# Kernel tuning notes

Hardware: AMD Instinct MI355X
Metric: run time of the kernel (lower is better)

## Reference

```python
import jax, jax.numpy as jnp
import numpy as np

BATCH, MAXLEN, EMB, HID = 64, 512, 1024, 1024


def setup_inputs() -> dict:
    key = jax.random.key(0)
    k1, k2, k3, k4 = jax.random.split(key, 4)
    stdv = 1.0 / np.sqrt(HID)  # matches reset_parameters uniform(-stdv, stdv)
    x = jax.random.normal(k1, (BATCH, MAXLEN, EMB), dtype=jnp.float32)
    lengths = jax.random.randint(k2, (BATCH,), 1, MAXLEN + 1)
    W_ih = jax.random.uniform(k3, (4 * HID, EMB), jnp.float32, -stdv, stdv)
    W_hh = jax.random.uniform(k4, (4 * HID, HID), jnp.float32, -stdv, stdv)
    return {"x": x, "lengths": lengths, "W_ih": W_ih, "W_hh": W_hh}


def reference(x, lengths, W_ih, W_hh):
    B, T, D = x.shape
    H = W_hh.shape[1]
    # length_to_mask: (B, T) float mask
    masks = (jnp.arange(T)[None, :] < lengths[:, None]).astype(x.dtype)
    # Hoist the input projection (no sequential dependency): (B, T, 4H)
    gi_all = jnp.einsum('btd,gd->btg', x, W_ih)

    def step(carry, inp):
        h, c = carry
        gi, m, is_init = inp  # gi: (B,4H), m: (B,), is_init: scalar bool
        gh = h @ W_hh.T  # (B, 4H)
        i_i, i_f, i_g, i_o = jnp.split(gi, 4, axis=1)
        h_i, h_f, h_g, h_o = jnp.split(gh, 4, axis=1)
        gx_i = jax.nn.sigmoid(i_i); fx_i = gx_i * (1 - gx_i)
        gx_f = jax.nn.sigmoid(i_f)
        gx_o = jax.nn.sigmoid(i_o); fx_o = gx_o * (1 - gx_o)
        gx_c = jnp.tanh(i_g);       fx_c = 1 - gx_c ** 2
        g_c = gx_i * gx_c
        g_c_tanh = jnp.tanh(g_c)
        g_h = gx_o * g_c_tanh
        Bt = gx_f * c
        Dt = gx_c * fx_i * h_i + gx_i * fx_c * h_g
        sech2 = 1 - g_c_tanh ** 2
        Et = gx_o * sech2 * gx_f * c
        Ft = gx_o * sech2 * Dt + fx_o * g_c_tanh * h_o
        h_new = Et + Ft + jnp.where(is_init, g_h, jnp.zeros_like(g_h))
        c_new = Bt + Dt + jnp.where(is_init, g_c, jnp.zeros_like(g_c))
        mm = m[:, None]
        h2 = h_new * mm + h * (1 - mm)
        c2 = c_new * mm + c * (1 - mm)
        return (h2, c2), h2

    h0 = jnp.zeros((B, H), x.dtype)
    c0 = jnp.zeros((B, H), x.dtype)
    xs = (gi_all.transpose(1, 0, 2),  # (T, B, 4H)
          masks.T,                    # (T, B)
          jnp.arange(T) == 0)         # (T,) is_initial flags
    (h_final, c_final), seq = jax.lax.scan(step, (h0, c0), xs)
    f_seq = seq.transpose(1, 0, 2)  # (B, T, H)
    return f_seq, h_final
```

## Files before the change

### kernel.cpp

```cpp
#include <hip/hip_runtime.h>
#include <math.h>

#define BB_  64
#define TT_  512
#define DD_  1024
#define HH_  1024

__device__ __forceinline__ unsigned short bf_rte(float f) {
    unsigned u = __float_as_uint(f);
    return (unsigned short)((u + 0x7FFFu + ((u >> 16) & 1u)) >> 16);
}
__device__ __forceinline__ void bf_split(float f, unsigned short& h,
                                         unsigned short& l) {
    unsigned u = __float_as_uint(f);
    unsigned r = (u + 0x7FFFu + ((u >> 16) & 1u)) >> 16;
    h = (unsigned short)r;
    l = bf_rte(f - __uint_as_float(r << 16));
}
__device__ __forceinline__ uint4 pack8(float4 v0, float4 v1, bool lo) {
    float f[8] = {v0.x, v0.y, v0.z, v0.w, v1.x, v1.y, v1.z, v1.w};
    unsigned short s[8];
#pragma unroll
    for (int j = 0; j < 8; ++j) {
        unsigned short h, l;
        bf_split(f[j], h, l);
        s[j] = lo ? l : h;
    }
    uint4 r;
    r.x = (unsigned)s[0] | ((unsigned)s[1] << 16);
    r.y = (unsigned)s[2] | ((unsigned)s[3] << 16);
    r.z = (unsigned)s[4] | ((unsigned)s[5] << 16);
    r.w = (unsigned)s[6] | ((unsigned)s[7] << 16);
    return r;
}

typedef short bf16x8 __attribute__((ext_vector_type(8)));
typedef float f32x4 __attribute__((ext_vector_type(4)));

__global__ __launch_bounds__(256)
void gemm_bf16x3(const float* __restrict__ X,
                 const float* __restrict__ Wih,
                 float* __restrict__ C)
{
    __shared__ unsigned short As[128 * 64];
    __shared__ unsigned short Bs[128 * 64];
    const int tid = threadIdx.x;
    const size_t m0 = (size_t)blockIdx.y * 128;
    const size_t n0 = (size_t)blockIdx.x * 128;
    const int wave = tid >> 6, lane = tid & 63;
    const int wr = wave >> 1, wc = wave & 1;

    f32x4 acc[4][4];
#pragma unroll
    for (int i = 0; i < 4; ++i)
#pragma unroll
        for (int j = 0; j < 4; ++j)
#pragma unroll
            for (int r = 0; r < 4; ++r) acc[i][j][r] = 0.f;

    for (int ks = 0; ks < 48; ++ks) {
        const int seg = ks >> 4;
        const int kph = (ks & 15) << 6;
        const bool aLo = (seg == 2);
        const bool bLo = (seg == 1);
        uint4 ua[4], ub[4];
#pragma unroll
        for (int c = 0; c < 4; ++c) {
            int chunk = tid + c * 256;
            int row = chunk >> 3, kc = chunk & 7;
            const float* ap = X + (m0 + row) * 1024 + kph + kc * 8;
            ua[c] = pack8(*(const float4*)ap, *(const float4*)(ap + 4), aLo);
            const float* bp = Wih + (n0 + row) * 1024 + kph + kc * 8;
            ub[c] = pack8(*(const float4*)bp, *(const float4*)(bp + 4), bLo);
        }
        __syncthreads();
#pragma unroll
        for (int c = 0; c < 4; ++c) {
            int chunk = tid + c * 256;
            int row = chunk >> 3, kc = chunk & 7;
            int sc = kc ^ (row & 7);
            *(uint4*)&As[row * 64 + sc * 8] = ua[c];
            *(uint4*)&Bs[row * 64 + sc * 8] = ub[c];
        }
        __syncthreads();
#pragma unroll
        for (int kk = 0; kk < 64; kk += 32) {
            bf16x8 af[4], bfv[4];
            const int ch = (kk >> 3) + (lane >> 4);
#pragma unroll
            for (int i = 0; i < 4; ++i) {
                int arow = wr * 64 + i * 16 + (lane & 15);
                af[i] = *(const bf16x8*)&As[arow * 64 + (ch ^ (arow & 7)) * 8];
                int brow = wc * 64 + i * 16 + (lane & 15);
                bfv[i] = *(const bf16x8*)&Bs[brow * 64 + (ch ^ (brow & 7)) * 8];
            }
#pragma unroll
            for (int i = 0; i < 4; ++i)
#pragma unroll
                for (int j = 0; j < 4; ++j)
                    acc[i][j] = __builtin_amdgcn_mfma_f32_16x16x32_bf16(
                        af[i], bfv[j], acc[i][j], 0, 0, 0);
        }
        __syncthreads();
    }
#pragma unroll
    for (int i = 0; i < 4; ++i) {
        size_t mrow = m0 + wr * 64 + i * 16 + (lane >> 4) * 4;
#pragma unroll
        for (int j = 0; j < 4; ++j) {
            size_t ncol = n0 + wc * 64 + j * 16 + (lane & 15);
            float* cp = C + mrow * 4096 + ncol;
            cp[0]        = acc[i][j][0];
            cp[4096]     = acc[i][j][1];
            cp[2 * 4096] = acc[i][j][2];
            cp[3 * 4096] = acc[i][j][3];
        }
    }
}

__global__ __launch_bounds__(256)
void gemm_nt_f32(const float* __restrict__ A, long lda, int M,
                 const float* __restrict__ Bw,
                 float* __restrict__ C, long ldc)
{
    __shared__ __align__(16) float As[16][132];
    __shared__ __align__(16) float Bs[16][132];
    const int tid = threadIdx.x;
    const long m0 = (long)blockIdx.x * 128;
    const long n0 = (long)blockIdx.y * 128;
    const int tx = tid & 15, ty = tid >> 4;
    const int sr = tid >> 2, sc = (tid & 3) << 2;
    float acc[8][8];
#pragma unroll
    for (int i = 0; i < 8; ++i)
#pragma unroll
        for (int j = 0; j < 8; ++j) acc[i][j] = 0.f;
    for (int k0 = 0; k0 < 1024; k0 += 16) {
#pragma unroll
        for (int rr = 0; rr < 2; ++rr) {
            long arow = m0 + sr + rr * 64;
            float4 v = make_float4(0.f, 0.f, 0.f, 0.f);
            if ((int)arow < M) v = *(const float4*)(A + arow * lda + k0 + sc);
            As[sc + 0][sr + rr * 64] = v.x; As[sc + 1][sr + rr * 64] = v.y;
            As[sc + 2][sr + rr * 64] = v.z; As[sc + 3][sr + rr * 64] = v.w;
            long bcol = n0 + sr + rr * 64;
            float4 w = *(const float4*)(Bw + bcol * 1024 + k0 + sc);
            Bs[sc + 0][sr + rr * 64] = w.x; Bs[sc + 1][sr + rr * 64] = w.y;
            Bs[sc + 2][sr + rr * 64] = w.z; Bs[sc + 3][sr + rr * 64] = w.w;
        }
        __syncthreads();
#pragma unroll
        for (int k = 0; k < 16; ++k) {
            float4 a0 = *(const float4*)&As[k][ty * 8];
            float4 a1 = *(const float4*)&As[k][ty * 8 + 4];
            float4 b0 = *(const float4*)&Bs[k][tx * 8];
            float4 b1 = *(const float4*)&Bs[k][tx * 8 + 4];
            float av[8] = {a0.x, a0.y, a0.z, a0.w, a1.x, a1.y, a1.z, a1.w};
            float bv[8] = {b0.x, b0.y, b0.z, b0.w, b1.x, b1.y, b1.z, b1.w};
#pragma unroll
            for (int i = 0; i < 8; ++i)
#pragma unroll
                for (int j = 0; j < 8; ++j) acc[i][j] += av[i] * bv[j];
        }
        __syncthreads();
    }
#pragma unroll
    for (int i = 0; i < 8; ++i) {
        long row = m0 + ty * 8 + i;
        if ((int)row < M) {
            *(float4*)(C + row * ldc + n0 + tx * 8) =
                make_float4(acc[i][0], acc[i][1], acc[i][2], acc[i][3]);
            *(float4*)(C + row * ldc + n0 + tx * 8 + 4) =
                make_float4(acc[i][4], acc[i][5], acc[i][6], acc[i][7]);
        }
    }
}

__global__ __launch_bounds__(512)
void lstm_step(const float4* __restrict__ h_in,
               float4* __restrict__ h_out,
               float* __restrict__ cbuf,
               const float* __restrict__ gi,
               long gstride,
               const float* __restrict__ Whh,
               const int* __restrict__ lengths,
               float* __restrict__ seq,
               int t)
{
    __shared__ float Ws[12][1024];
    __shared__ float red[8][12][66];
    __shared__ float gix[4][4][68];

    const int tid  = threadIdx.x;
    const int h0   = blockIdx.x << 2;
    const int wave = tid >> 6;
    const int lane = tid & 63;

#pragma unroll
    for (int it = 0; it < 6; ++it) {
        int i = tid + it * 512;
        int r = i >> 8;
        int k4 = i & 255;
        int q = r >> 2, hl = r & 3;
        int grow = (q == 0) ? (h0 + hl) : (q == 1) ? (2048 + h0 + hl)
                                                   : (3072 + h0 + hl);
        *(float4*)&Ws[r][k4 * 4] =
            *(const float4*)(Whh + (size_t)grow * 1024 + k4 * 4);
    }

    if (tid < 256) {
        const int pb = tid >> 2, pg = tid & 3;
        const float4 gv = *reinterpret_cast<const float4*>(
            gi + (long)pb * gstride + pg * 1024 + h0);
        gix[pg][0][pb] = gv.x;
        gix[pg][1][pb] = gv.y;
        gix[pg][2][pb] = gv.z;
        gix[pg][3][pb] = gv.w;
    }
    __syncthreads();

    float acc[12];
#pragma unroll
    for (int r = 0; r < 12; ++r) acc[r] = 0.f;
    const int k4b = wave << 5;
    const float4* hq = h_in + (size_t)k4b * 64 + lane;
#pragma unroll 4
    for (int k4 = 0; k4 < 32; ++k4) {
        float4 hv = hq[(size_t)k4 * 64];
        const int kc = (k4b + k4) << 2;
#pragma unroll
        for (int r = 0; r < 12; ++r) {
            float4 wv = *(const float4*)&Ws[r][kc];
            acc[r] += hv.x * wv.x + hv.y * wv.y + hv.z * wv.z + hv.w * wv.w;
        }
    }
#pragma unroll
    for (int r = 0; r < 12; ++r) red[wave][r][lane] = acc[r];
    __syncthreads();

    if (tid < 256) {
        const int cb = tid >> 2;
        const int hl = tid & 3;
        float h_i = 0.f, h_g = 0.f, h_o = 0.f;
#pragma unroll
        for (int w = 0; w < 8; ++w) {
            h_i += red[w][0 + hl][cb];
            h_g += red[w][4 + hl][cb];
            h_o += red[w][8 + hl][cb];
        }
        float i_i = gix[0][hl][cb];
        float i_f = gix[1][hl][cb];
        float i_g = gix[2][hl][cb];
        float i_o = gix[3][hl][cb];

        float gx_i = 1.f / (1.f + expf(-i_i));
        float fx_i = gx_i * (1.f - gx_i);
        float gx_f = 1.f / (1.f + expf(-i_f));
        float gx_o = 1.f / (1.f + expf(-i_o));
        float fx_o = gx_o * (1.f - gx_o);
        float gx_c = tanhf(i_g);
        float fx_c = 1.f - gx_c * gx_c;
        float g_c  = gx_i * gx_c;
        float g_ct = tanhf(g_c);
        float g_h  = gx_o * g_ct;

        float c_old = cbuf[(size_t)(h0 + hl) * 64 + cb];
        float Bt = gx_f * c_old;
        float Dt = gx_c * fx_i * h_i + gx_i * fx_c * h_g;
        float sech2 = 1.f - g_ct * g_ct;
        float Et = gx_o * sech2 * gx_f * c_old;
        float Ft = gx_o * sech2 * Dt + fx_o * g_ct * h_o;

        float h_new = Et + Ft + ((t == 0) ? g_h : 0.f);
        float c_new = Bt + Dt + ((t == 0) ? g_c : 0.f);

        float hprev = ((const float*)h_in)[(size_t)blockIdx.x * 256 + tid];
        bool msk = (t < lengths[cb]);
        float h2 = msk ? h_new : hprev;
        float c2 = msk ? c_new : c_old;

        cbuf[(size_t)(h0 + hl) * 64 + cb] = c2;
        ((float*)h_out)[(size_t)blockIdx.x * 256 + tid] = h2;
        seq[(size_t)cb * (TT_ * HH_) + (size_t)t * HH_ + h0 + hl] = h2;
    }
}

__global__ void zero_hc(float* __restrict__ hbuf0, float* __restrict__ cb)
{
    int i = blockIdx.x * 256 + threadIdx.x;
    hbuf0[i] = 0.f;
    cb[i]    = 0.f;
}

__global__ void h_final_k(const float* __restrict__ hbuf,
                          float* __restrict__ outf)
{
    int b = blockIdx.x;
    for (int h = threadIdx.x; h < 1024; h += 256)
        outf[(size_t)b * 1024 + h] =
            hbuf[(size_t)(h >> 2) * 256 + b * 4 + (h & 3)];
}

extern "C" void kernel_launch(void* const* d_in, const int* in_sizes, int n_in,
                              void* d_out, int out_size, void* d_ws, size_t ws_size,
                              hipStream_t stream)
{
    const float* x   = (const float*)d_in[0];
    const int*   len = (const int*)d_in[1];
    const float* Wih = (const float*)d_in[2];
    const float* Whh = (const float*)d_in[3];
    float* out = (float*)d_out;

    float* hbase = (float*)d_ws;
    float* cb    = hbase + 2 * 65536;
    float* gi    = hbase + 3 * 65536;

    const size_t needA = (size_t)3 * 65536 * 4 + (size_t)32768 * 4096 * 4;
    const bool pathA = (ws_size >= needA);

    zero_hc<<<dim3(256), dim3(256), 0, stream>>>(hbase, cb);

    if (pathA) {
        gemm_bf16x3<<<dim3(32, 256), dim3(256), 0, stream>>>(x, Wih, gi);
    }

    for (int t = 0; t < 512; ++t) {
        const float* gstep;
        long gstride;
        if (pathA) {
            gstep = gi + (size_t)t * 4096;
            gstride = (long)TT_ * 4096;
        } else {
            gemm_nt_f32<<<dim3(1, 32), dim3(256), 0, stream>>>(
                x + (size_t)t * 1024, (long)TT_ * 1024, 64, Wih, gi, 4096);
            gstep = gi;
            gstride = 4096;
        }
        const float4* hin  = (const float4*)(hbase + (t & 1) * 65536);
        float4*       hout = (float4*)(hbase + ((t + 1) & 1) * 65536);
        lstm_step<<<dim3(256), dim3(512), 0, stream>>>(
            hin, hout, cb, gstep, gstride, Whh, len, out, t);
    }

    h_final_k<<<dim3(64), dim3(256), 0, stream>>>(
        hbase, out + (size_t)BB_ * TT_ * HH_);
}
```

Baseline: 13.91 ms.

## Replace per-step LSTM launches with persistent cooperative kernel and grid barrier

Runs the 512-step recurrence inside one cooperative kernel of 256 blocks. Each block keeps its W_hh slice in shared memory across all steps, and h and c stay in registers. A two-level atomic grid barrier separates timesteps, which removes 512 kernel launches and the repeated reload of the weight slice. The cost is reliance on spin barriers and co-residency of all blocks with 1024 threads each. The barrier has a spin cap that could silently break synchronisation if it is hit.

```diff
diff --git a/kernel.cpp b/kernel.cpp
--- a/kernel.cpp
+++ b/kernel.cpp
@@ -116,6 +116,152 @@
             cp[3 * 4096] = acc[i][j][3];
         }
     }
+}
+
+__global__ __launch_bounds__(1024, 4)
+void lstm_persist2(const float* __restrict__ Whh,
+                   const float* __restrict__ gi,
+                   const int* __restrict__ lengths,
+                   float* __restrict__ hbuf,
+                   unsigned* __restrict__ bar,
+                   float* __restrict__ seq,
+                   float* __restrict__ hfin)
+{
+    __shared__ float Ws[12][1024];
+    __shared__ float red[16][12][66];
+
+    const int tid  = threadIdx.x;
+    const int bid  = blockIdx.x;
+    const int h0   = bid << 2;
+    const int wave = tid >> 6;
+    const int lane = tid & 63;
+    const int cb   = tid >> 2;
+    const int hl   = tid & 3;
+
+    for (int i = tid; i < 12 * 256; i += 1024) {
+        int r = i >> 8, k4 = i & 255;
+        int q = r >> 2, rhl = r & 3;
+        int grow = (q == 0) ? (h0 + rhl) : (q == 1) ? (2048 + h0 + rhl)
+                                                    : (3072 + h0 + rhl);
+        *(float4*)&Ws[r][k4 * 4] =
+            *(const float4*)(Whh + (size_t)grow * 1024 + k4 * 4);
+    }
+
+    float h_reg = 0.f, c_reg = 0.f;
+    int len_b = 0;
+    size_t gi_base = 0;
+    if (tid < 256) {
+        len_b = lengths[cb];
+        gi_base = ((size_t)cb * TT_) * 4096 + h0 + hl;
+    }
+    __syncthreads();
+
+    for (int t = 0; t < TT_; ++t) {
+        const float* hin = hbuf + (t & 1) * 65536;
+
+        float gv0 = 0.f, gv1 = 0.f, gv2 = 0.f, gv3 = 0.f;
+        if (tid < 256) {
+            const float* gp = gi + gi_base + (size_t)t * 4096;
+            gv0 = gp[0]; gv1 = gp[1024]; gv2 = gp[2048]; gv3 = gp[3072];
+        }
+
+        float acc[12];
+#pragma unroll
+        for (int r = 0; r < 12; ++r) acc[r] = 0.f;
+        const int kb = wave << 6;
+        const float* hp = hin + (size_t)kb * 64 + lane;
+
+        float hv0[16], hv1[16];
+#pragma unroll
+        for (int e = 0; e < 16; ++e)
+            hv0[e] = __hip_atomic_load(hp + (size_t)e * 64,
+                                       __ATOMIC_RELAXED, __HIP_MEMORY_SCOPE_AGENT);
+#pragma unroll
+        for (int c2 = 0; c2 < 4; ++c2) {
+            float* cur = (c2 & 1) ? hv1 : hv0;
+            float* nxt = (c2 & 1) ? hv0 : hv1;
+            if (c2 < 3) {
+                const float* np = hp + (size_t)(c2 + 1) * 16 * 64;
+#pragma unroll
+                for (int e = 0; e < 16; ++e)
+                    nxt[e] = __hip_atomic_load(np + (size_t)e * 64,
+                                               __ATOMIC_RELAXED, __HIP_MEMORY_SCOPE_AGENT);
+            }
+#pragma unroll
+            for (int kk = 0; kk < 4; ++kk) {
+                const int kcol = kb + c2 * 16 + kk * 4;
+#pragma unroll
+                for (int r = 0; r < 12; ++r) {
+                    const float4 wv = *(const float4*)&Ws[r][kcol];
+                    acc[r] += cur[kk * 4 + 0] * wv.x + cur[kk * 4 + 1] * wv.y
+                            + cur[kk * 4 + 2] * wv.z + cur[kk * 4 + 3] * wv.w;
+                }
+            }
+        }
+#pragma unroll
+        for (int r = 0; r < 12; ++r) red[wave][r][lane] = acc[r];
+        __syncthreads();
+
+        if (tid < 256) {
+            float h_i = 0.f, h_g = 0.f, h_o = 0.f;
+#pragma unroll
+            for (int w = 0; w < 16; ++w) {
+                h_i += red[w][0 + hl][cb];
+                h_g += red[w][4 + hl][cb];
+                h_o += red[w][8 + hl][cb];
+            }
+            float gx_i = 1.f / (1.f + expf(-gv0));
+            float fx_i = gx_i * (1.f - gx_i);
+            float gx_f = 1.f / (1.f + expf(-gv1));
+            float gx_o = 1.f / (1.f + expf(-gv3));
+            float fx_o = gx_o * (1.f - gx_o);
+            float gx_c = tanhf(gv2);
+            float fx_c = 1.f - gx_c * gx_c;
+            float g_c  = gx_i * gx_c;
+            float g_ct = tanhf(g_c);
+            float g_h  = gx_o * g_ct;
+
+            float Bt = gx_f * c_reg;
+            float Dt = gx_c * fx_i * h_i + gx_i * fx_c * h_g;
+            float sech2 = 1.f - g_ct * g_ct;
+            float Et = gx_o * sech2 * gx_f * c_reg;
+            float Ft = gx_o * sech2 * Dt + fx_o * g_ct * h_o;
+
+            float h_new = Et + Ft + ((t == 0) ? g_h : 0.f);
+            float c_new = Bt + Dt + ((t == 0) ? g_c : 0.f);
+
+            bool msk = (t < len_b);
+            h_reg = msk ? h_new : h_reg;
+            c_reg = msk ? c_new : c_reg;
+
+            seq[(size_t)cb * (TT_ * HH_) + (size_t)t * HH_ + h0 + hl] = h_reg;
+            float* hnext = hbuf + ((t + 1) & 1) * 65536;
+            __hip_atomic_store(hnext + (size_t)(h0 + hl) * 64 + cb, h_reg,
+                               __ATOMIC_RELAXED, __HIP_MEMORY_SCOPE_AGENT);
+        }
+
+        asm volatile("s_waitcnt vmcnt(0)" ::: "memory");
+        __syncthreads();
+        if (tid == 0) {
+            const unsigned g = (unsigned)(bid & 7);
+            unsigned pos = __hip_atomic_fetch_add(&bar[g * 32], 1u,
+                               __ATOMIC_ACQ_REL, __HIP_MEMORY_SCOPE_AGENT);
+            if (pos == 32u * (unsigned)(t + 1) - 1u) {
+                __hip_atomic_fetch_add(&bar[256], 1u,
+                               __ATOMIC_ACQ_REL, __HIP_MEMORY_SCOPE_AGENT);
+            }
+            const unsigned target = 8u * (unsigned)(t + 1);
+            int spins = 0;
+            while (__hip_atomic_load(&bar[256], __ATOMIC_ACQUIRE,
+                                     __HIP_MEMORY_SCOPE_AGENT) < target) {
+                if (++spins > 1000000) break;
+                __builtin_amdgcn_s_sleep(1);
+            }
+        }
+        __syncthreads();
+    }
+
+    if (tid < 256) hfin[(size_t)cb * HH_ + h0 + hl] = h_reg;
 }
 
 __global__ __launch_bounds__(256)
@@ -180,12 +326,10 @@
 void lstm_step(const float4* __restrict__ h_in,
                float4* __restrict__ h_out,
                float* __restrict__ cbuf,
-               const float* __restrict__ gi,
-               long gstride,
+               const float* __restrict__ gi, long gstride,
                const float* __restrict__ Whh,
                const int* __restrict__ lengths,
-               float* __restrict__ seq,
-               int t)
+               float* __restrict__ seq, int t)
 {
     __shared__ float Ws[12][1024];
     __shared__ float red[8][12][66];
@@ -199,23 +343,19 @@
 #pragma unroll
     for (int it = 0; it < 6; ++it) {
         int i = tid + it * 512;
-        int r = i >> 8;
-        int k4 = i & 255;
+        int r = i >> 8, k4 = i & 255;
         int q = r >> 2, hl = r & 3;
         int grow = (q == 0) ? (h0 + hl) : (q == 1) ? (2048 + h0 + hl)
                                                    : (3072 + h0 + hl);
         *(float4*)&Ws[r][k4 * 4] =
             *(const float4*)(Whh + (size_t)grow * 1024 + k4 * 4);
     }
-
     if (tid < 256) {
         const int pb = tid >> 2, pg = tid & 3;
         const float4 gv = *reinterpret_cast<const float4*>(
             gi + (long)pb * gstride + pg * 1024 + h0);
-        gix[pg][0][pb] = gv.x;
-        gix[pg][1][pb] = gv.y;
-        gix[pg][2][pb] = gv.z;
-        gix[pg][3][pb] = gv.w;
+        gix[pg][0][pb] = gv.x; gix[pg][1][pb] = gv.y;
+        gix[pg][2][pb] = gv.z; gix[pg][3][pb] = gv.w;
     }
     __syncthreads();
 
@@ -248,11 +388,8 @@
             h_g += red[w][4 + hl][cb];
             h_o += red[w][8 + hl][cb];
         }
-        float i_i = gix[0][hl][cb];
-        float i_f = gix[1][hl][cb];
-        float i_g = gix[2][hl][cb];
-        float i_o = gix[3][hl][cb];
-
+        float i_i = gix[0][hl][cb], i_f = gix[1][hl][cb];
+        float i_g = gix[2][hl][cb], i_o = gix[3][hl][cb];
         float gx_i = 1.f / (1.f + expf(-i_i));
         float fx_i = gx_i * (1.f - gx_i);
         float gx_f = 1.f / (1.f + expf(-i_f));
@@ -263,33 +400,27 @@
         float g_c  = gx_i * gx_c;
         float g_ct = tanhf(g_c);
         float g_h  = gx_o * g_ct;
-
         float c_old = cbuf[(size_t)(h0 + hl) * 64 + cb];
         float Bt = gx_f * c_old;
         float Dt = gx_c * fx_i * h_i + gx_i * fx_c * h_g;
         float sech2 = 1.f - g_ct * g_ct;
         float Et = gx_o * sech2 * gx_f * c_old;
         float Ft = gx_o * sech2 * Dt + fx_o * g_ct * h_o;
-
         float h_new = Et + Ft + ((t == 0) ? g_h : 0.f);
         float c_new = Bt + Dt + ((t == 0) ? g_c : 0.f);
-
         float hprev = ((const float*)h_in)[(size_t)blockIdx.x * 256 + tid];
         bool msk = (t < lengths[cb]);
         float h2 = msk ? h_new : hprev;
         float c2 = msk ? c_new : c_old;
-
         cbuf[(size_t)(h0 + hl) * 64 + cb] = c2;
         ((float*)h_out)[(size_t)blockIdx.x * 256 + tid] = h2;
         seq[(size_t)cb * (TT_ * HH_) + (size_t)t * HH_ + h0 + hl] = h2;
     }
 }
 
-__global__ void zero_hc(float* __restrict__ hbuf0, float* __restrict__ cb)
-{
-    int i = blockIdx.x * 256 + threadIdx.x;
-    hbuf0[i] = 0.f;
-    cb[i]    = 0.f;
+__global__ void zero_ws(float* __restrict__ p)
+{
+    p[blockIdx.x * 256 + threadIdx.x] = 0.f;
 }
 
 __global__ void h_final_k(const float* __restrict__ hbuf,
@@ -312,36 +443,34 @@
     float* out = (float*)d_out;
 
     float* hbase = (float*)d_ws;
-    float* cb    = hbase + 2 * 65536;
+    float* reg2  = hbase + 2 * 65536;
     float* gi    = hbase + 3 * 65536;
 
-    const size_t needA = (size_t)3 * 65536 * 4 + (size_t)32768 * 4096 * 4;
+    const size_t needA = ((size_t)3 * 65536 + (size_t)32768 * 4096) * 4;
     const bool pathA = (ws_size >= needA);
 
-    zero_hc<<<dim3(256), dim3(256), 0, stream>>>(hbase, cb);
+    zero_ws<<<dim3(768), dim3(256), 0, stream>>>(hbase);
+
+    float* seqp = out;
+    float* hfin = out + (size_t)BB_ * TT_ * HH_;
 
     if (pathA) {
         gemm_bf16x3<<<dim3(32, 256), dim3(256), 0, stream>>>(x, Wih, gi);
-    }
-
-    for (int t = 0; t < 512; ++t) {
-        const float* gstep;
-        long gstride;
-        if (pathA) {
-            gstep = gi + (size_t)t * 4096;
-            gstride = (long)TT_ * 4096;
-        } else {
+        unsigned* bar = (unsigned*)reg2;
+        void* args[] = {(void*)&Whh, (void*)&gi, (void*)&len,
+                        (void*)&hbase, (void*)&bar, (void*)&seqp, (void*)&hfin};
+        hipLaunchCooperativeKernel((void*)lstm_persist2, dim3(256), dim3(1024),
+                                   args, 0, stream);
+    } else {
+        float* cbuf = reg2;
+        for (int t = 0; t < 512; ++t) {
             gemm_nt_f32<<<dim3(1, 32), dim3(256), 0, stream>>>(
                 x + (size_t)t * 1024, (long)TT_ * 1024, 64, Wih, gi, 4096);
-            gstep = gi;
-            gstride = 4096;
-        }
-        const float4* hin  = (const float4*)(hbase + (t & 1) * 65536);
-        float4*       hout = (float4*)(hbase + ((t + 1) & 1) * 65536);
-        lstm_step<<<dim3(256), dim3(512), 0, stream>>>(
-            hin, hout, cb, gstep, gstride, Whh, len, out, t);
-    }
-
-    h_final_k<<<dim3(64), dim3(256), 0, stream>>>(
-        hbase, out + (size_t)BB_ * TT_ * HH_);
-}
+            const float4* hin  = (const float4*)(hbase + (t & 1) * 65536);
+            float4*       hout = (float4*)(hbase + ((t + 1) & 1) * 65536);
+            lstm_step<<<dim3(256), dim3(512), 0, stream>>>(
+                hin, hout, cbuf, gi, 4096, Whh, len, out, t);
+        }
+        h_final_k<<<dim3(64), dim3(256), 0, stream>>>(hbase, hfin);
+    }
+}
```

After: 15.69 ms. 1.13x slower.
